# Optimization experiments

Measured on AMD Instinct MI355X. Metric: run time of the kernel, lower is better.

## Reference

```python
import jax, jax.numpy as jnp
import numpy as np

B, S, D_IN, H, D_HEAD = 4, 1024, 768, 12, 64


def setup_inputs() -> dict:
    key = jax.random.key(0)
    k1, k2, k3, k4 = jax.random.split(key, 4)
    x = jax.random.normal(k1, (B, S, D_IN), dtype=jnp.float32)
    # Per-head projection weights stored as [H, d_in, d_head] (equivalent to
    # nn.Linear weight [d_head, d_in] applied as x @ W.T), scaled like default init.
    scale = 1.0 / np.sqrt(D_IN)
    Wq = jax.random.normal(k2, (H, D_IN, D_HEAD), dtype=jnp.float32) * scale
    Wk = jax.random.normal(k3, (H, D_IN, D_HEAD), dtype=jnp.float32) * scale
    Wv = jax.random.normal(k4, (H, D_IN, D_HEAD), dtype=jnp.float32) * scale
    return {"x": x, "Wq": Wq, "Wk": Wk, "Wv": Wv}


def reference(x, Wq, Wk, Wv):
    # Vectorized over heads; faithful to per-head causal attention then concat.
    q = jnp.einsum("bsd,hde->bhse", x, Wq)  # [B,H,S,Dh]
    k = jnp.einsum("bsd,hde->bhse", x, Wk)
    v = jnp.einsum("bsd,hde->bhse", x, Wv)
    scale = 1.0 / jnp.sqrt(jnp.asarray(D_HEAD, dtype=q.dtype))
    scores = jnp.einsum("bhse,bhte->bhst", q, k) * scale  # [B,H,S,S]
    causal = jnp.tril(jnp.ones((S, S), dtype=bool))
    scores = jnp.where(causal, scores, jnp.finfo(scores.dtype).min)
    attn = jax.nn.softmax(scores, axis=-1)  # dropout p=0.0 (eval) -> identity
    ctx = jnp.einsum("bhst,bhte->bhse", attn, v)  # [B,H,S,Dh]
    # concat heads along last dim: [B,S,H*Dh]
    return jnp.transpose(ctx, (0, 2, 1, 3)).reshape(B, S, H * D_HEAD)
```

## Files before the change

### kernel.cpp

```cpp
#include <hip/hip_runtime.h>
#include <hip/hip_bf16.h>

#define NB 4
#define SS 1024
#define DIN 768
#define NH 12
#define DH 64

typedef float f32x4 __attribute__((ext_vector_type(4)));
typedef short bf16x8 __attribute__((ext_vector_type(8)));

static __device__ __forceinline__ unsigned short f2bf(float f) {
    __hip_bfloat16 h = __float2bfloat16(f);
    return *reinterpret_cast<unsigned short*>(&h);
}

static __device__ __forceinline__ float exp2_fast(float x) {
    return __builtin_amdgcn_exp2f(x);
}

static __device__ __forceinline__ void gload16(const void* g, void* l) {
    __builtin_amdgcn_global_load_lds(
        (const __attribute__((address_space(1))) void*)g,
        (__attribute__((address_space(3))) void*)l, 16, 0, 0);
}

__global__ void prep_kernel(const float* __restrict__ x, const float* __restrict__ Wq,
                            const float* __restrict__ Wk, const float* __restrict__ Wv,
                            unsigned short* __restrict__ xb, unsigned short* __restrict__ wt) {
    __shared__ float lds[64][68];
    int bid = blockIdx.x, tid = threadIdx.x;
    {
        int i = (bid * 256 + tid) * 4;
        float4 v = *reinterpret_cast<const float4*>(x + i);
        ushort4 o;
        o.x = f2bf(v.x); o.y = f2bf(v.y); o.z = f2bf(v.z); o.w = f2bf(v.w);
        *reinterpret_cast<ushort4*>(xb + i) = o;
    }
    if (bid < 432) {
        int d0 = (bid % 12) * 64, h = (bid / 12) % 12, p = bid / 144;
        const float* W = (p == 0) ? Wq : (p == 1) ? Wk : Wv;
        const float* base = W + (size_t)h * DIN * DH;
        int rr = tid >> 4, c4 = tid & 15;
#pragma unroll
        for (int i = 0; i < 4; ++i) {
            int d = i * 16 + rr;
            float4 v = *reinterpret_cast<const float4*>(base + (size_t)(d0 + d) * DH + c4 * 4);
            lds[d][c4 * 4 + 0] = v.x; lds[d][c4 * 4 + 1] = v.y;
            lds[d][c4 * 4 + 2] = v.z; lds[d][c4 * 4 + 3] = v.w;
        }
        __syncthreads();
        unsigned short* outp = wt + ((size_t)(p * NH + h) * DH) * DIN;
#pragma unroll
        for (int i = 0; i < 4; ++i) {
            int e = i * 16 + rr;
            int dc = c4 * 4;
            ushort4 o;
            o.x = f2bf(lds[dc + 0][e]); o.y = f2bf(lds[dc + 1][e]);
            o.z = f2bf(lds[dc + 2][e]); o.w = f2bf(lds[dc + 3][e]);
            *reinterpret_cast<ushort4*>(outp + (size_t)e * DIN + d0 + dc) = o;
        }
    }
}

__global__ __launch_bounds__(256) void qkv_gemm_kernel(
    const unsigned short* __restrict__ xb, const unsigned short* __restrict__ wt,
    unsigned short* __restrict__ qb, unsigned short* __restrict__ kb,
    unsigned short* __restrict__ vT) {
    __shared__ __align__(16) unsigned char smem[28672];
    unsigned short* a_lds = (unsigned short*)smem;
    unsigned short* b_lds = (unsigned short*)(smem + 16384);

    int sb = (blockIdx.x & 7) * 96 + (blockIdx.x >> 3);
    int m0 = (sb & 31) * 128;
    int n0 = (sb >> 5) * 96;
    int tid = threadIdx.x, lane = tid & 63, w = tid >> 6;
    int l15 = lane & 15, hi4 = (lane >> 4) * 4, hi8 = (lane >> 4) * 8;
    int wr = w >> 1, wc = w & 1;
    int srow = tid >> 3;
    int scolb = (tid & 7) * 16;
    int sw = (l15 & 7) << 4;

    f32x4 acc[4][3] = {};

    for (int k0 = 0; k0 < DIN; k0 += 64) {
        __syncthreads();
#pragma unroll
        for (int i = 0; i < 4; ++i) {
            int row = i * 32 + srow;
            int cb = scolb ^ ((row & 7) << 4);
            gload16(xb + (size_t)(m0 + row) * DIN + k0 + (cb >> 1), a_lds + row * 64 + (scolb >> 1));
        }
#pragma unroll
        for (int i = 0; i < 3; ++i) {
            int row = i * 32 + srow;
            int cb = scolb ^ ((row & 7) << 4);
            gload16(wt + (size_t)(n0 + row) * DIN + k0 + (cb >> 1), b_lds + row * 64 + (scolb >> 1));
        }
        __syncthreads();
#pragma unroll
        for (int kk = 0; kk < 64; kk += 32) {
            int cb = ((kk + hi8) * 2) ^ sw;
            bf16x8 af[4], bfr[3];
#pragma unroll
            for (int m = 0; m < 4; ++m)
                af[m] = *reinterpret_cast<const bf16x8*>(a_lds + (wr * 64 + m * 16 + l15) * 64 + (cb >> 1));
#pragma unroll
            for (int n = 0; n < 3; ++n)
                bfr[n] = *reinterpret_cast<const bf16x8*>(b_lds + (wc * 48 + n * 16 + l15) * 64 + (cb >> 1));
#pragma unroll
            for (int m = 0; m < 4; ++m)
#pragma unroll
                for (int n = 0; n < 3; ++n)
                    acc[m][n] = __builtin_amdgcn_mfma_f32_16x16x32_bf16(af[m], bfr[n], acc[m][n], 0, 0, 0);
        }
    }
    __syncthreads();

    int p  = n0 / 768;
    int cp = (n0 % 768) + wc * 48;
    int b  = m0 >> 10;
    int s_base = (m0 & 1023) + wr * 64;

    if (p < 2) {
        float qs = (p == 0) ? 0.180336880f : 1.0f;
        unsigned short* dstb = (p == 0) ? qb : kb;
#pragma unroll
        for (int m = 0; m < 4; ++m)
#pragma unroll
            for (int n = 0; n < 3; ++n)
#pragma unroll
                for (int r = 0; r < 4; ++r) {
                    int col = cp + n * 16 + l15;
                    int h = col >> 6, e = col & 63;
                    dstb[((size_t)(b * NH + h) * SS + s_base + m * 16 + hi4 + r) * DH + e] =
                        f2bf(acc[m][n][r] * qs);
                }
    } else {
        float* sc = (float*)smem + w * 784;
#pragma unroll
        for (int m = 0; m < 4; ++m) {
#pragma unroll
            for (int n = 0; n < 3; ++n)
#pragma unroll
                for (int r = 0; r < 4; ++r)
                    sc[(hi4 + r) * 49 + n * 16 + l15] = acc[m][n][r];
            if (lane < 48) {
                unsigned short vv[16];
#pragma unroll
                for (int t2 = 0; t2 < 16; ++t2) vv[t2] = f2bf(sc[t2 * 49 + lane]);
                int col = cp + lane;
                int h = col >> 6, e = col & 63;
                unsigned short* dst = vT + ((size_t)(b * NH + h) * DH + e) * SS + s_base + m * 16;
                *reinterpret_cast<uint4*>(dst)     = *reinterpret_cast<const uint4*>(vv);
                *reinterpret_cast<uint4*>(dst + 8) = *reinterpret_cast<const uint4*>(vv + 8);
            }
        }
    }
}

struct AttnCtx {
    const unsigned short* kg;
    const unsigned short* vg;
    char* smem;
    unsigned short* pw;
    int srow, scolb, l15, hi, sw;
};

static __device__ __forceinline__ void attn_stage(const AttnCtx& c, int buf, int kv) {
    unsigned short* kl = (unsigned short*)(c.smem + buf * 8192);
    unsigned short* vl = (unsigned short*)(c.smem + 16384 + buf * 8192);
#pragma unroll
    for (int i = 0; i < 2; ++i) {
        int row = i * 32 + c.srow;
        int cb = c.scolb ^ ((row & 7) << 4);
        gload16(c.kg + (size_t)(kv * 64 + row) * DH + (cb >> 1), kl + row * 64 + (c.scolb >> 1));
        gload16(c.vg + (size_t)row * SS + kv * 64 + (cb >> 1),   vl + row * 64 + (c.scolb >> 1));
    }
}

template<bool DIAG>
static __device__ __forceinline__ void attn_step(
    const AttnCtx& c, int buf, int kv, int qg,
    bf16x8 qf0, bf16x8 qf1, float& m_r, float& l_r, f32x4 o_acc[4]) {
    const unsigned short* kl = (const unsigned short*)(c.smem + buf * 8192);
    const unsigned short* vl = (const unsigned short*)(c.smem + 16384 + buf * 8192);
    int l15 = c.l15, hi = c.hi, sw = c.sw;
    int hi4 = hi * 4, hi8 = hi * 8;

    f32x4 sacc[4] = {};
    __builtin_amdgcn_s_setprio(1);
#pragma unroll
    for (int s = 0; s < 2; ++s) {
        int cb = ((32 * s + hi8) * 2) ^ sw;
#pragma unroll
        for (int n = 0; n < 4; ++n) {
            bf16x8 kf = *reinterpret_cast<const bf16x8*>(kl + (16 * n + l15) * 64 + (cb >> 1));
            sacc[n] = __builtin_amdgcn_mfma_f32_16x16x32_bf16(kf, s == 0 ? qf0 : qf1, sacc[n], 0, 0, 0);
        }
    }
    __builtin_amdgcn_s_setprio(0);

    float pv[4][4];
#pragma unroll
    for (int n = 0; n < 4; ++n)
#pragma unroll
        for (int r = 0; r < 4; ++r) {
            float sv = sacc[n][r];
            if (DIAG && (kv * 64 + 16 * n + hi4 + r) > qg) sv = -INFINITY;
            pv[n][r] = sv;
        }

    float mn[4];
#pragma unroll
    for (int n = 0; n < 4; ++n)
        mn[n] = fmaxf(fmaxf(pv[n][0], pv[n][1]), fmaxf(pv[n][2], pv[n][3]));
    float mx = fmaxf(fmaxf(mn[0], mn[1]), fmaxf(mn[2], mn[3]));
    mx = fmaxf(mx, __shfl_xor(mx, 16));
    mx = fmaxf(mx, __shfl_xor(mx, 32));

    if (!__all(mx - m_r <= 8.0f)) {
        float m_new = fmaxf(m_r, mx);
        float alpha = exp2_fast(m_r - m_new);
        l_r *= alpha;
#pragma unroll
        for (int n = 0; n < 4; ++n)
#pragma unroll
            for (int r = 0; r < 4; ++r) o_acc[n][r] *= alpha;
        m_r = m_new;
    }
    float sn[4];
#pragma unroll
    for (int n = 0; n < 4; ++n) {
#pragma unroll
        for (int r = 0; r < 4; ++r) pv[n][r] = exp2_fast(pv[n][r] - m_r);
        sn[n] = (pv[n][0] + pv[n][1]) + (pv[n][2] + pv[n][3]);
    }
    float sum = (sn[0] + sn[1]) + (sn[2] + sn[3]);
    sum += __shfl_xor(sum, 16);
    sum += __shfl_xor(sum, 32);
    l_r += sum;

    int xr = (l15 & 7) * 4;
    unsigned int* pwu = (unsigned int*)c.pw;
#pragma unroll
    for (int n = 0; n < 4; ++n)
#pragma unroll
        for (int p2 = 0; p2 < 2; ++p2) {
            unsigned int w32 = (unsigned int)f2bf(pv[n][2 * p2]) |
                               ((unsigned int)f2bf(pv[n][2 * p2 + 1]) << 16);
            pwu[l15 * 32 + ((8 * n + 2 * hi + p2) ^ xr)] = w32;
        }
    int i0 = (4 * hi) ^ xr;
    int i1 = (16 + 4 * hi) ^ xr;
    bf16x8 pa0 = *reinterpret_cast<const bf16x8*>(c.pw + l15 * 64 + i0 * 2);
    bf16x8 pa1 = *reinterpret_cast<const bf16x8*>(c.pw + l15 * 64 + i1 * 2);

    __builtin_amdgcn_s_setprio(1);
#pragma unroll
    for (int s = 0; s < 2; ++s) {
        int cb = ((32 * s + hi8) * 2) ^ sw;
#pragma unroll
        for (int n = 0; n < 4; ++n) {
            bf16x8 vf = *reinterpret_cast<const bf16x8*>(vl + (16 * n + l15) * 64 + (cb >> 1));
            o_acc[n] = __builtin_amdgcn_mfma_f32_16x16x32_bf16(vf, s == 0 ? pa0 : pa1, o_acc[n], 0, 0, 0);
        }
    }
    __builtin_amdgcn_s_setprio(0);
}

__global__ __launch_bounds__(256, 4) void attn_kernel(
    const unsigned short* __restrict__ qb, const unsigned short* __restrict__ kb,
    const unsigned short* __restrict__ vT, float* __restrict__ out) {
    __shared__ __align__(16) char smem[40960];

    int bid = blockIdx.x;
    int qi = 15 - bid / 48;
    int rem = bid % 48;
    int h = rem % 12, b = rem / 12;
    int q0 = qi * 64;
    int tid = threadIdx.x, lane = tid & 63, w = tid >> 6;
    int l15 = lane & 15, hi = lane >> 4;
    int hi4 = hi * 4, hi8 = hi * 8;
    size_t bh = (size_t)(b * NH + h);

    AttnCtx c;
    c.kg = kb + bh * SS * DH;
    c.vg = vT + bh * DH * SS;
    c.smem = smem;
    c.pw = (unsigned short*)(smem + 32768) + w * 1024;
    c.srow = tid >> 3; c.scolb = (tid & 7) * 16;
    c.l15 = l15; c.hi = hi; c.sw = (l15 & 7) << 4;

    int qg = q0 + 16 * w + l15;
    const unsigned short* qp = qb + (bh * SS + qg) * DH;
    bf16x8 qf0 = *reinterpret_cast<const bf16x8*>(qp + hi8);
    bf16x8 qf1 = *reinterpret_cast<const bf16x8*>(qp + 32 + hi8);

    float m_r = -INFINITY, l_r = 0.f;
    f32x4 o_acc[4] = {};

    attn_stage(c, 0, 0);
    __syncthreads();
    for (int kv = 0; kv < qi; ++kv) {
        attn_stage(c, (kv & 1) ^ 1, kv + 1);
        attn_step<false>(c, kv & 1, kv, qg, qf0, qf1, m_r, l_r, o_acc);
        __syncthreads();
    }
    attn_step<true>(c, qi & 1, qi, qg, qf0, qf1, m_r, l_r, o_acc);
    __syncthreads();

    float inv = 1.f / l_r;
    float* sc = (float*)(smem + w * 4352);
#pragma unroll
    for (int n = 0; n < 4; ++n)
#pragma unroll
        for (int r = 0; r < 4; ++r)
            sc[l15 * 68 + 16 * n + hi4 + r] = o_acc[n][r] * inv;
    __builtin_amdgcn_s_waitcnt(0);
#pragma unroll
    for (int j = 0; j < 4; ++j) {
        f32x4 v = *reinterpret_cast<const f32x4*>(sc + l15 * 68 + j * 16 + hi4);
        *reinterpret_cast<f32x4*>(out + ((size_t)b * SS + q0 + 16 * w + l15) * (NH * DH)
                                  + h * DH + j * 16 + hi4) = v;
    }
}

extern "C" void kernel_launch(void* const* d_in, const int* in_sizes, int n_in,
                              void* d_out, int out_size, void* d_ws, size_t ws_size,
                              hipStream_t stream) {
    const float* x  = (const float*)d_in[0];
    const float* Wq = (const float*)d_in[1];
    const float* Wk = (const float*)d_in[2];
    const float* Wv = (const float*)d_in[3];
    float* out = (float*)d_out;

    char* ws = (char*)d_ws;
    unsigned short* xb = (unsigned short*)ws;
    unsigned short* wt = (unsigned short*)(ws +  6291456);
    unsigned short* qb = (unsigned short*)(ws +  9830400);
    unsigned short* kb = (unsigned short*)(ws + 16121856);
    unsigned short* vT = (unsigned short*)(ws + 22413312);

    hipLaunchKernelGGL(prep_kernel,     dim3(3072), dim3(256), 0, stream, x, Wq, Wk, Wv, xb, wt);
    hipLaunchKernelGGL(qkv_gemm_kernel, dim3(768),  dim3(256), 0, stream, xb, wt, qb, kb, vT);
    hipLaunchKernelGGL(attn_kernel,     dim3(768),  dim3(256), 0, stream, qb, kb, vT, out);
}
```

Before: 116.2 us.

## Double-buffer QKV GEMM LDS tiles and remap attention block-to-work order

The QKV projection GEMM now double-buffers its A/B tiles in LDS, so the next K-slice is issued while the current one feeds the MFMAs. This removes one barrier per iteration and overlaps global loads with compute, at the cost of doubling LDS per block (which may lower occupancy). The attention kernel's block index mapping is also rearranged so that long causal rows are paired with short ones across the dispatch order, aiming for better load balance across CUs.

```diff
diff --git a/kernel.cpp b/kernel.cpp
--- a/kernel.cpp
+++ b/kernel.cpp
@@ -67,9 +67,7 @@
     const unsigned short* __restrict__ xb, const unsigned short* __restrict__ wt,
     unsigned short* __restrict__ qb, unsigned short* __restrict__ kb,
     unsigned short* __restrict__ vT) {
-    __shared__ __align__(16) unsigned char smem[28672];
-    unsigned short* a_lds = (unsigned short*)smem;
-    unsigned short* b_lds = (unsigned short*)(smem + 16384);
+    __shared__ __align__(16) unsigned char smem[57344];
 
     int sb = (blockIdx.x & 7) * 96 + (blockIdx.x >> 3);
     int m0 = (sb & 31) * 128;
@@ -83,21 +81,30 @@
 
     f32x4 acc[4][3] = {};
 
-    for (int k0 = 0; k0 < DIN; k0 += 64) {
-        __syncthreads();
+    auto stage = [&](int buf, int k0) {
+        unsigned short* al = (unsigned short*)(smem + buf * 16384);
+        unsigned short* bl = (unsigned short*)(smem + 32768 + buf * 12288);
 #pragma unroll
         for (int i = 0; i < 4; ++i) {
             int row = i * 32 + srow;
             int cb = scolb ^ ((row & 7) << 4);
-            gload16(xb + (size_t)(m0 + row) * DIN + k0 + (cb >> 1), a_lds + row * 64 + (scolb >> 1));
+            gload16(xb + (size_t)(m0 + row) * DIN + k0 + (cb >> 1), al + row * 64 + (scolb >> 1));
         }
 #pragma unroll
         for (int i = 0; i < 3; ++i) {
             int row = i * 32 + srow;
             int cb = scolb ^ ((row & 7) << 4);
-            gload16(wt + (size_t)(n0 + row) * DIN + k0 + (cb >> 1), b_lds + row * 64 + (scolb >> 1));
-        }
-        __syncthreads();
+            gload16(wt + (size_t)(n0 + row) * DIN + k0 + (cb >> 1), bl + row * 64 + (scolb >> 1));
+        }
+    };
+
+    stage(0, 0);
+    __syncthreads();
+    for (int t = 0; t < 12; ++t) {
+        int cur = t & 1;
+        if (t < 11) stage(cur ^ 1, (t + 1) * 64);
+        const unsigned short* a_lds = (const unsigned short*)(smem + cur * 16384);
+        const unsigned short* b_lds = (const unsigned short*)(smem + 32768 + cur * 12288);
 #pragma unroll
         for (int kk = 0; kk < 64; kk += 32) {
             int cb = ((kk + hi8) * 2) ^ sw;
@@ -114,8 +121,8 @@
                 for (int n = 0; n < 3; ++n)
                     acc[m][n] = __builtin_amdgcn_mfma_f32_16x16x32_bf16(af[m], bfr[n], acc[m][n], 0, 0, 0);
         }
-    }
-    __syncthreads();
+        __syncthreads();
+    }
 
     int p  = n0 / 768;
     int cp = (n0 % 768) + wc * 48;
@@ -275,9 +282,11 @@
     __shared__ __align__(16) char smem[40960];
 
     int bid = blockIdx.x;
-    int qi = 15 - bid / 48;
-    int rem = bid % 48;
-    int h = rem % 12, b = rem / 12;
+    int cc = bid & 255, j = bid >> 8;
+    int u = cc >> 4, v = cc & 15;
+    int qi = (j == 0) ? u : ((j == 1) ? 15 - (u >> 1) : 7 - (u >> 1));
+    int idx = (j == 0) ? v : (16 + 16 * (u & 1) + v);
+    int h = idx % 12, b = idx / 12;
     int q0 = qi * 64;
     int tid = threadIdx.x, lane = tid & 63, w = tid >> 6;
     int l15 = lane & 15, hi = lane >> 4;
@@ -319,10 +328,10 @@
             sc[l15 * 68 + 16 * n + hi4 + r] = o_acc[n][r] * inv;
     __builtin_amdgcn_s_waitcnt(0);
 #pragma unroll
-    for (int j = 0; j < 4; ++j) {
-        f32x4 v = *reinterpret_cast<const f32x4*>(sc + l15 * 68 + j * 16 + hi4);
+    for (int jj = 0; jj < 4; ++jj) {
+        f32x4 vv = *reinterpret_cast<const f32x4*>(sc + l15 * 68 + jj * 16 + hi4);
         *reinterpret_cast<f32x4*>(out + ((size_t)b * SS + q0 + 16 * w + l15) * (NH * DH)
-                                  + h * DH + j * 16 + hi4) = v;
+                                  + h * DH + jj * 16 + hi4) = vv;
     }
 }
 
```

After: 119.5 us. 2.8% more time.
